# Kernel tuning notes

Measured on AMD Instinct MI355X. Metric: run time of the kernel, lower is better.

Reference implementation:

```python
import jax, jax.numpy as jnp
import numpy as np

N = 50000      # nodes
E = 800000     # edges (avg degree 16)
G = 8          # graphs in batch
D = 128        # in/hidden feats
C = 10         # classes


def setup_inputs() -> dict:
    key = jax.random.key(0)
    ks = jax.random.split(key, 9)
    x = jax.random.normal(ks[0], (N, D), dtype=jnp.float32)
    edge_index = jax.random.randint(ks[1], (2, E), 0, N)
    node2graph = jnp.sort(jax.random.randint(ks[2], (N,), 0, G))
    s = 1.0 / np.sqrt(D)
    W1 = jax.random.normal(ks[3], (D, D), dtype=jnp.float32) * s
    b1 = jnp.zeros((D,), jnp.float32)
    W2 = jax.random.normal(ks[4], (D, D), dtype=jnp.float32) * s
    b2 = jnp.zeros((D,), jnp.float32)
    Wl = jax.random.normal(ks[5], (D, C), dtype=jnp.float32) * s
    bl = jnp.zeros((C,), jnp.float32)
    return {"x": x, "edge_index": edge_index, "node2graph": node2graph,
            "W1": W1, "b1": b1, "W2": W2, "b2": b2, "Wl": Wl, "bl": bl}


def _graph_conv(h, src, dst, out_isqrt, in_isqrt, W, b):
    # DGL GraphConv, norm='both': D_in^{-1/2} A D_out^{-1/2} (h W) + b
    h = (h * out_isqrt[:, None]) @ W
    agg = jax.ops.segment_sum(h[src], dst, num_segments=N)  # SpMM gather/scatter
    return agg * in_isqrt[:, None] + b


def reference(x, edge_index, node2graph, W1, b1, W2, b2, Wl, bl):
    src, dst = edge_index[0], edge_index[1]
    ones_e = jnp.ones((E,), jnp.float32)
    out_deg = jnp.clip(jax.ops.segment_sum(ones_e, src, num_segments=N), 1.0)
    in_deg = jnp.clip(jax.ops.segment_sum(ones_e, dst, num_segments=N), 1.0)
    out_isqrt = jax.lax.rsqrt(out_deg)
    in_isqrt = jax.lax.rsqrt(in_deg)

    h = jax.nn.relu(_graph_conv(x, src, dst, out_isqrt, in_isqrt, W1, b1))
    h = jax.nn.relu(_graph_conv(h, src, dst, out_isqrt, in_isqrt, W2, b2))

    # AvgPooling: per-graph mean of node features
    sums = jax.ops.segment_sum(h, node2graph, num_segments=G)
    counts = jnp.clip(jax.ops.segment_sum(jnp.ones((N,), jnp.float32), node2graph, num_segments=G), 1.0)
    hg = sums / counts[:, None]

    logits = hg @ Wl + bl
    return jax.nn.softmax(logits, axis=1)
```

## Files before the change

### kernel.cpp

```cpp
#include <hip/hip_runtime.h>
#include <stdint.h>

#define FD 128
#define NG 8
#define NC 10
#define MAXB 1024
#define CHUNK 4096
#define BFPAD 16

typedef __attribute__((ext_vector_type(8))) short bf16x8;
typedef __attribute__((ext_vector_type(4))) float f32x4;
typedef __attribute__((ext_vector_type(2))) float f32x2;

__device__ __forceinline__ float bf2f(uint16_t u){
    union { uint32_t i; float f; } v; v.i = ((uint32_t)u) << 16; return v.f;
}
__device__ __forceinline__ uint16_t f2bf(float f){
    union { float f; uint32_t i; } v; v.f = f;
    uint32_t r = v.i + 0x7fff + ((v.i >> 16) & 1);
    return (uint16_t)(r >> 16);
}

#if __has_builtin(__builtin_amdgcn_cvt_pk_f32_fp8) && __has_builtin(__builtin_amdgcn_cvt_pk_fp8_f32)
__device__ __forceinline__ f32x2 fp8lo2f(uint32_t p){
    return __builtin_amdgcn_cvt_pk_f32_fp8((int)p, false);
}
__device__ __forceinline__ f32x2 fp8hi2f(uint32_t p){
    return __builtin_amdgcn_cvt_pk_f32_fp8((int)p, true);
}
__device__ __forceinline__ uint32_t pk4fp8(float a, float b, float c, float d){
    int u = 0;
    u = __builtin_amdgcn_cvt_pk_fp8_f32(a, b, u, false);
    u = __builtin_amdgcn_cvt_pk_fp8_f32(c, d, u, true);
    return (uint32_t)u;
}
#else
__device__ __forceinline__ float fp8tof(uint32_t b){
    union { uint32_t i; float f; } v;
    v.i = ((b & 0x7f) << 20) | ((b & 0x80) << 24);
    return v.f * 0x1p120f;
}
__device__ __forceinline__ f32x2 fp8lo2f(uint32_t p){
    return (f32x2){fp8tof(p & 0xff), fp8tof((p >> 8) & 0xff)};
}
__device__ __forceinline__ f32x2 fp8hi2f(uint32_t p){
    return (f32x2){fp8tof((p >> 16) & 0xff), fp8tof((p >> 24) & 0xff)};
}
__device__ __forceinline__ uint32_t f2fp8(float f){
    union { float f; uint32_t i; } v; v.f = f;
    uint32_t s = (v.i >> 24) & 0x80;
    float a = fabsf(f);
    if (a < 0x1p-10f) return s;
    if (a > 448.f) return s | 0x7e;
    v.f = a;
    uint32_t r = v.i + 0x7ffff + ((v.i >> 20) & 1);
    int e = (int)(r >> 23) - 127 + 7;
    uint32_t m = (r >> 20) & 7;
    if (e <= 0){
        uint32_t q = (uint32_t)(a * 512.f + 0.5f);
        return s | (q > 7 ? 8 : q);
    }
    if (e > 15) return s | 0x7e;
    return s | ((uint32_t)e << 3) | m;
}
__device__ __forceinline__ uint32_t pk4fp8(float a, float b, float c, float d){
    return (uint32_t)f2fp8(a) | ((uint32_t)f2fp8(b)<<8) |
           ((uint32_t)f2fp8(c)<<16) | ((uint32_t)f2fp8(d)<<24);
}
#endif

__global__ __launch_bounds__(256) void k_prep(const float* __restrict__ W1,
        const float* __restrict__ W2, uint16_t* Wf1, uint16_t* Wf2,
        int N, int B, int* __restrict__ deg_out, int* __restrict__ bucket_fill,
        float* __restrict__ pool){
    int t = threadIdx.x;
    int id = blockIdx.x*256 + t;
    {
        int w = id >> 14;
        int r = id & 16383;
        int j = r & 7, frag = r >> 3;
        int lane = frag & 63, t2 = frag >> 6;
        int n = t2 & 7, kk = t2 >> 3;
        int k = kk*32 + (lane>>4)*8 + j;
        int col = n*16 + (lane&15);
        float v = (w ? W2 : W1)[k*128 + col];
        (w ? Wf2 : Wf1)[r] = f2bf(v);
    }
    for (int i = id; i < N; i += 32768) deg_out[i] = 0;
    for (int i = id; i < B*BFPAD; i += 32768) bucket_fill[i] = 0;
    if (id < NG*FD) pool[id] = 0.f;
}

__global__ __launch_bounds__(1024) void k_gemm_scatter(const int* __restrict__ ei,
        int E, int B, int shift, int CAP, int C,
        int* __restrict__ bucket_fill, int* __restrict__ deg_out,
        uint32_t* __restrict__ tempD,
        const float* __restrict__ X, const uint16_t* __restrict__ Wf,
        uint8_t* __restrict__ out8, int N){
    int t = threadIdx.x;
    if (blockIdx.x < C){
        __shared__ int hc[MAXB];
        __shared__ int hb_[MAXB];
        int c = blockIdx.x;
        for (int i=t;i<B;i+=1024) hc[i]=0;
        __syncthreads();
        int e0 = c*CHUNK, e1 = min(E, e0+CHUNK);
        int ss[4], dd[4], pl[4];
        #pragma unroll
        for (int k=0;k<4;k++){
            int e = e0 + t + k*1024;
            bool ok = e < e1;
            int s = ok ? ei[e]   : 0;
            int d = ok ? ei[E+e] : -1;
            ss[k] = s; dd[k] = d; pl[k] = 0;
            if (ok){
                pl[k] = atomicAdd(&hc[d>>shift], 1);
                atomicAdd(&deg_out[s], 1);
            }
        }
        __syncthreads();
        for (int i=t;i<B;i+=1024){
            int cn = hc[i];
            hb_[i] = cn ? atomicAdd(&bucket_fill[i*BFPAD], cn) : 0;
        }
        __syncthreads();
        int lmask = (1<<shift) - 1;
        #pragma unroll
        for (int k=0;k<4;k++){
            int d = dd[k];
            if (d >= 0){
                int b = d >> shift;
                int p = hb_[b] + pl[k];
                if (p < CAP)
                    tempD[(size_t)b*CAP + p] = ((uint32_t)(d & lmask) << 20) | (uint32_t)ss[k];
            }
        }
        return;
    }
    int wave = t>>6, lane = t&63, quad = lane>>4, low = lane&15;
    int rowA  = (blockIdx.x - C)*256 + wave*16 + low;
    int rowAc = min(rowA, N-1);
    const float* arow = X + (size_t)rowAc*FD;
    bf16x8 ah[4];
    #pragma unroll
    for (int kk=0;kk<4;kk++){
        f32x4 f0 = *(const f32x4*)(arow + kk*32 + quad*8);
        f32x4 f1 = *(const f32x4*)(arow + kk*32 + quad*8 + 4);
        #pragma unroll
        for (int j=0;j<4;j++) ah[kk][j]   = (short)f2bf(f0[j]);
        #pragma unroll
        for (int j=0;j<4;j++) ah[kk][j+4] = (short)f2bf(f1[j]);
    }
    f32x4 acc[8];
    #pragma unroll
    for (int n=0;n<8;n++) acc[n] = (f32x4){0.f,0.f,0.f,0.f};
    #pragma unroll
    for (int kk=0;kk<4;kk++){
        #pragma unroll
        for (int n=0;n<8;n++){
            bf16x8 bh = *(const bf16x8*)(Wf + ((size_t)((kk*8+n)*64 + lane))*8);
            acc[n] = __builtin_amdgcn_mfma_f32_16x16x32_bf16(bh, ah[kk], acc[n], 0, 0, 0);
        }
    }
    if (rowA < N){
        uint8_t* orow = out8 + (size_t)rowA*FD;
        #pragma unroll
        for (int n=0;n<8;n++){
            uint32_t pk = pk4fp8(acc[n][0], acc[n][1], acc[n][2], acc[n][3]);
            *(uint32_t*)(orow + n*16 + quad*4) = pk;
        }
    }
}

__global__ __launch_bounds__(256) void k_build(const uint32_t* __restrict__ tempD,
        const int* __restrict__ bucket_fill, const int* __restrict__ deg_out,
        int B, int shift, int N, int CAP,
        int* __restrict__ row_off, int* __restrict__ deg_in,
        float* __restrict__ isqo, int* __restrict__ csr){
    __shared__ int cnt_[MAXB];
    __shared__ int off_[MAXB];
    int b = blockIdx.x, t = threadIdx.x;
    int range = 1<<shift, nb0 = b<<shift;
    int fill = min(bucket_fill[b*BFPAD], CAP);
    const uint32_t* seg = tempD + (size_t)b*CAP;
    for (int i=t;i<range;i+=256) cnt_[i]=0;
    __syncthreads();
    for (int i=t;i<fill;i+=256)
        atomicAdd(&cnt_[seg[i]>>20], 1);
    __syncthreads();
    if (range == 64){
        if (t < 64){
            int v = cnt_[t];
            int inc = v;
            #pragma unroll
            for (int o=1;o<64;o<<=1){
                int u = __shfl_up(inc, o);
                if (t >= o) inc += u;
            }
            off_[t] = inc - v;
        }
    } else if (t == 0){
        int run = 0;
        for (int i=0;i<range;i++){ off_[i]=run; run+=cnt_[i]; }
    }
    __syncthreads();
    int base = b*CAP;
    for (int i=t;i<range;i+=256){
        int node = nb0 + i;
        if (node < N){
            row_off[node] = base + off_[i];
            deg_in[node]  = cnt_[i];
            isqo[node]    = rsqrtf((float)max(deg_out[node], 1));
        }
    }
    __syncthreads();
    int* csrb = csr + (size_t)base;
    for (int i=t;i<fill;i+=256){
        uint32_t v = seg[i];
        int p = atomicAdd(&off_[v>>20], 1);
        csrb[p] = (int)(v & 0xFFFFFu);
    }
}

__device__ __forceinline__ void spmm_row(const uint2* __restrict__ tp,
        const int* __restrict__ csr_src, const float* __restrict__ isqo,
        int e0, int e1, int l, int qb,
        f32x2& a01, f32x2& a23, f32x2& a45, f32x2& a67){
    for (int base = e0; base < e1; base += 16){
        int my = 0;
        if (base + l < e1) my = csr_src[base + l];
        int cnt = min(16, e1 - base);
        for (int j0 = 0; j0 < cnt; j0 += 8){
            int ss[8];
            #pragma unroll
            for (int k=0;k<8;k++)
                ss[k] = __shfl(my, qb + min(j0 + k, cnt-1));
            uint2 p[8]; float w[8];
            #pragma unroll
            for (int k=0;k<8;k++)
                p[k] = tp[(size_t)ss[k]*16 + l];
            #pragma unroll
            for (int k=0;k<8;k++)
                w[k] = isqo[ss[k]];
            #pragma unroll
            for (int k=0;k<8;k++){
                if (j0 + k < cnt){
                    a01 += fp8lo2f(p[k].x)*w[k]; a23 += fp8hi2f(p[k].x)*w[k];
                    a45 += fp8lo2f(p[k].y)*w[k]; a67 += fp8hi2f(p[k].y)*w[k];
                }
            }
        }
    }
}

__global__ __launch_bounds__(256) void k_spmm_gemm(const uint8_t* __restrict__ tmp8,
        const int* __restrict__ row_off, const int* __restrict__ deg_in,
        const int* __restrict__ csr_src, const float* __restrict__ isqo,
        const float* __restrict__ bias, const uint16_t* __restrict__ Wf,
        uint8_t* __restrict__ out8, int N){
    __shared__ __align__(16) uint16_t hsrow[64][136];
    int tid = threadIdx.x;
    int l = tid & 15, qid = tid >> 4, qb = (tid & 63) & 48;
    const uint2* tp = (const uint2*)tmp8;
    f32x4 bv0 = *(const f32x4*)(bias + l*8);
    f32x4 bv1 = *(const f32x4*)(bias + l*8 + 4);
    #pragma unroll
    for (int i = 0; i < 4; i++){
        int rowL = qid*4 + i;
        int node = blockIdx.x*64 + rowL;
        int e0 = 0, e1 = 0;
        if (node < N){ e0 = row_off[node]; e1 = e0 + deg_in[node]; }
        f32x2 a01={0.f,0.f}, a23={0.f,0.f}, a45={0.f,0.f}, a67={0.f,0.f};
        spmm_row(tp, csr_src, isqo, e0, e1, l, qb, a01, a23, a45, a67);
        float isq = rsqrtf((float)max(e1 - e0, 1));
        float r0 = fmaxf(a01.x*isq + bv0[0], 0.f);
        float r1 = fmaxf(a01.y*isq + bv0[1], 0.f);
        float r2 = fmaxf(a23.x*isq + bv0[2], 0.f);
        float r3 = fmaxf(a23.y*isq + bv0[3], 0.f);
        float r4 = fmaxf(a45.x*isq + bv1[0], 0.f);
        float r5 = fmaxf(a45.y*isq + bv1[1], 0.f);
        float r6 = fmaxf(a67.x*isq + bv1[2], 0.f);
        float r7 = fmaxf(a67.y*isq + bv1[3], 0.f);
        uint4 o;
        o.x = (uint32_t)f2bf(r0) | ((uint32_t)f2bf(r1) << 16);
        o.y = (uint32_t)f2bf(r2) | ((uint32_t)f2bf(r3) << 16);
        o.z = (uint32_t)f2bf(r4) | ((uint32_t)f2bf(r5) << 16);
        o.w = (uint32_t)f2bf(r6) | ((uint32_t)f2bf(r7) << 16);
        if (node >= N) o = (uint4){0u,0u,0u,0u};
        *(uint4*)(&hsrow[rowL][l*8]) = o;
    }
    __syncthreads();
    int wave = tid>>6, lane = tid&63, quad = lane>>4, low = lane&15;
    int rowL = wave*16 + low;
    int rowA = blockIdx.x*64 + rowL;
    bf16x8 ah[4];
    #pragma unroll
    for (int kk=0;kk<4;kk++)
        ah[kk] = *(const bf16x8*)(&hsrow[rowL][kk*32 + quad*8]);
    f32x4 acc[8];
    #pragma unroll
    for (int n=0;n<8;n++) acc[n] = (f32x4){0.f,0.f,0.f,0.f};
    #pragma unroll
    for (int kk=0;kk<4;kk++){
        #pragma unroll
        for (int n=0;n<8;n++){
            bf16x8 bh = *(const bf16x8*)(Wf + ((size_t)((kk*8+n)*64 + lane))*8);
            acc[n] = __builtin_amdgcn_mfma_f32_16x16x32_bf16(bh, ah[kk], acc[n], 0, 0, 0);
        }
    }
    if (rowA < N){
        uint8_t* orow = out8 + (size_t)rowA*FD;
        #pragma unroll
        for (int n=0;n<8;n++){
            uint32_t pk = pk4fp8(acc[n][0], acc[n][1], acc[n][2], acc[n][3]);
            *(uint32_t*)(orow + n*16 + quad*4) = pk;
        }
    }
}

__global__ __launch_bounds__(256) void k_spmm_pool(const uint8_t* __restrict__ tmp8,
        const int* __restrict__ row_off, const int* __restrict__ deg_in,
        const int* __restrict__ csr_src, const float* __restrict__ isqo,
        const float* __restrict__ bias, const int* __restrict__ n2g,
        float* __restrict__ pool, int N){
    __shared__ float sacc[NG*FD];
    int tid = threadIdx.x;
    for (int i = tid; i < NG*FD; i += 256) sacc[i] = 0.f;
    __syncthreads();
    int l = tid & 15, qid = tid >> 4, qb = (tid & 63) & 48;
    const uint2* tp = (const uint2*)tmp8;
    f32x4 bv0 = *(const f32x4*)(bias + l*8);
    f32x4 bv1 = *(const f32x4*)(bias + l*8 + 4);
    int rg = -1;
    float racc[8];
    #pragma unroll
    for (int j=0;j<8;j++) racc[j] = 0.f;
    #pragma unroll
    for (int i = 0; i < 4; i++){
        int node = blockIdx.x*64 + qid*4 + i;
        if (node < N){
            int e0 = row_off[node], e1 = e0 + deg_in[node];
            f32x2 a01={0.f,0.f}, a23={0.f,0.f}, a45={0.f,0.f}, a67={0.f,0.f};
            spmm_row(tp, csr_src, isqo, e0, e1, l, qb, a01, a23, a45, a67);
            float isq = rsqrtf((float)max(e1 - e0, 1));
            float r[8];
            r[0] = fmaxf(a01.x*isq + bv0[0], 0.f);
            r[1] = fmaxf(a01.y*isq + bv0[1], 0.f);
            r[2] = fmaxf(a23.x*isq + bv0[2], 0.f);
            r[3] = fmaxf(a23.y*isq + bv0[3], 0.f);
            r[4] = fmaxf(a45.x*isq + bv1[0], 0.f);
            r[5] = fmaxf(a45.y*isq + bv1[1], 0.f);
            r[6] = fmaxf(a67.x*isq + bv1[2], 0.f);
            r[7] = fmaxf(a67.y*isq + bv1[3], 0.f);
            int g = n2g[node];
            if (g != rg){
                if (rg >= 0){
                    #pragma unroll
                    for (int j=0;j<8;j++) atomicAdd(&sacc[rg*FD + l*8 + j], racc[j]);
                }
                rg = g;
                #pragma unroll
                for (int j=0;j<8;j++) racc[j] = 0.f;
            }
            #pragma unroll
            for (int j=0;j<8;j++) racc[j] += r[j];
        }
    }
    if (rg >= 0){
        #pragma unroll
        for (int j=0;j<8;j++) atomicAdd(&sacc[rg*FD + l*8 + j], racc[j]);
    }
    __syncthreads();
    for (int i = tid; i < NG*FD; i += 256){
        float v = sacc[i];
        if (v != 0.f) atomicAdd(&pool[i], v);
    }
}

__global__ __launch_bounds__(128) void k_final(const float* __restrict__ pool,
        const int* __restrict__ n2g, int N, const float* __restrict__ Wl,
        const float* __restrict__ bl, float* __restrict__ out){
    __shared__ int ub[NG+1];
    __shared__ float logits[NG][NC];
    int t = threadIdx.x;
    if (t <= NG){
        int lo = 0, hi = N;
        while (lo < hi){ int mid = (lo+hi)>>1; if (n2g[mid] < t) lo = mid+1; else hi = mid; }
        ub[t] = lo;
    }
    __syncthreads();
    if (t < NG*NC){
        int g = t/NC, c = t%NC;
        float cnt = (float)max(ub[g+1]-ub[g], 1);
        float inv = 1.f/cnt;
        float acc = bl[c];
        for (int d=0; d<FD; d++)
            acc += pool[g*FD+d]*inv * Wl[d*NC+c];
        logits[g][c] = acc;
    }
    __syncthreads();
    if (t < NG*NC){
        int g = t/NC, c = t%NC;
        float m = -1e30f;
        for (int i=0;i<NC;i++) m = fmaxf(m, logits[g][i]);
        float ssum = 0.f;
        for (int i=0;i<NC;i++) ssum += expf(logits[g][i]-m);
        out[t] = expf(logits[g][c]-m)/ssum;
    }
}

extern "C" void kernel_launch(void* const* d_in, const int* in_sizes, int n_in,
                              void* d_out, int out_size, void* d_ws, size_t ws_size,
                              hipStream_t stream) {
    const float* x   = (const float*)d_in[0];
    const int*   ei  = (const int*)d_in[1];
    const int*   n2g = (const int*)d_in[2];
    const float* W1  = (const float*)d_in[3];
    const float* b1  = (const float*)d_in[4];
    const float* W2  = (const float*)d_in[5];
    const float* b2  = (const float*)d_in[6];
    const float* Wl  = (const float*)d_in[7];
    const float* bl  = (const float*)d_in[8];
    float* outp = (float*)d_out;

    int N = in_sizes[2];
    int E = in_sizes[1] / 2;

    int shift = 6;
    while ((((N + (1<<shift) - 1) >> shift) > MAXB) && shift < 10) shift++;
    int B = (N + (1<<shift) - 1) >> shift;
    int C = (E + CHUNK - 1) / CHUNK;
    int meanFill = (int)(((long long)E << shift) / (N > 0 ? N : 1)) + 1;
    int CAP = 4096;
    while (CAP < 4*meanFill) CAP <<= 1;

    char* w = (char*)d_ws;
    size_t off = 0;
    auto alloc = [&](size_t bytes)->char*{ char* p = w + off; off += (bytes + 255) & ~(size_t)255; return p; };
    float*    pool        = (float*)alloc((size_t)NG*FD*4);
    int*      deg_out     = (int*)alloc((size_t)N*4);
    int*      deg_in      = (int*)alloc((size_t)N*4);
    int*      row_off     = (int*)alloc((size_t)N*4);
    float*    isqo        = (float*)alloc((size_t)N*4);
    int*      bucket_fill = (int*)alloc((size_t)MAXB*BFPAD*4);
    uint16_t* Wf1         = (uint16_t*)alloc(16384*2);
    uint16_t* Wf2         = (uint16_t*)alloc(16384*2);
    uint32_t* tempD       = (uint32_t*)alloc((size_t)B*CAP*4);
    int*      csr         = (int*)alloc((size_t)B*CAP*4);
    uint8_t*  tmp8        = (uint8_t*)alloc((size_t)N*FD);
    uint8_t*  tmp8b       = (uint8_t*)alloc((size_t)N*FD);
    (void)ws_size;

    int gb2 = (N + 255)/256;
    int gb  = (N + 63)/64;

    k_prep        <<<128,      256,  0, stream>>>(W1, W2, Wf1, Wf2, N, B, deg_out, bucket_fill, pool);
    k_gemm_scatter<<<C + gb2,  1024, 0, stream>>>(ei, E, B, shift, CAP, C,
                                                  bucket_fill, deg_out, tempD,
                                                  x, Wf1, tmp8, N);
    k_build       <<<B,        256,  0, stream>>>(tempD, bucket_fill, deg_out, B, shift, N, CAP,
                                                  row_off, deg_in, isqo, csr);
    k_spmm_gemm   <<<gb,       256,  0, stream>>>(tmp8,  row_off, deg_in, csr, isqo, b1, Wf2, tmp8b, N);
    k_spmm_pool   <<<gb,       256,  0, stream>>>(tmp8b, row_off, deg_in, csr, isqo, b2, n2g, pool, N);
    k_final       <<<1,        128,  0, stream>>>(pool, n2g, N, Wl, bl, outp);
}
```

Measured before the change: 220.6 us.

## Stage edge buckets in LDS for coalesced writes; bucket out-degree via source buckets

Edge scatter blocks now group each chunk's edges by destination bucket in LDS with padded offsets and write them to global memory as 16-byte vectors, replacing scattered 4-byte writes. Out-degree counting moves from global atomics on deg_out to a second set of blocks that bucket 16-bit source-local IDs, which k_build then counts in LDS. The layer-2 out-degree normalisation is folded into the fp8 output of k_spmm_gemm, so k_spmm_pool skips the per-edge isqo gather. The cost is extra block-wide prefix scans with many syncthreads, padding sentinels that must be filtered, and a smaller CAP that raises the risk of bucket overflow.

```diff
diff --git a/kernel.cpp b/kernel.cpp
--- a/kernel.cpp
+++ b/kernel.cpp
@@ -6,7 +6,7 @@
 #define NC 10
 #define MAXB 1024
 #define CHUNK 4096
-#define BFPAD 16
+#define BFPAD 4
 
 typedef __attribute__((ext_vector_type(8))) short bf16x8;
 typedef __attribute__((ext_vector_type(4))) float f32x4;
@@ -71,7 +71,7 @@
 
 __global__ __launch_bounds__(256) void k_prep(const float* __restrict__ W1,
         const float* __restrict__ W2, uint16_t* Wf1, uint16_t* Wf2,
-        int N, int B, int* __restrict__ deg_out, int* __restrict__ bucket_fill,
+        int B, int* __restrict__ bfD, int* __restrict__ bfS,
         float* __restrict__ pool){
     int t = threadIdx.x;
     int id = blockIdx.x*256 + t;
@@ -86,59 +86,121 @@
         float v = (w ? W2 : W1)[k*128 + col];
         (w ? Wf2 : Wf1)[r] = f2bf(v);
     }
-    for (int i = id; i < N; i += 32768) deg_out[i] = 0;
-    for (int i = id; i < B*BFPAD; i += 32768) bucket_fill[i] = 0;
+    for (int i = id; i < B*BFPAD; i += 32768){ bfD[i] = 0; bfS[i] = 0; }
     if (id < NG*FD) pool[id] = 0.f;
 }
 
 __global__ __launch_bounds__(1024) void k_gemm_scatter(const int* __restrict__ ei,
         int E, int B, int shift, int CAP, int C,
-        int* __restrict__ bucket_fill, int* __restrict__ deg_out,
-        uint32_t* __restrict__ tempD,
+        int* __restrict__ bfD, int* __restrict__ bfS,
+        uint32_t* __restrict__ tempD, uint16_t* __restrict__ tempS,
         const float* __restrict__ X, const uint16_t* __restrict__ Wf,
         uint8_t* __restrict__ out8, int N){
+    __shared__ __align__(16) char lds[45056];
     int t = threadIdx.x;
-    if (blockIdx.x < C){
-        __shared__ int hc[MAXB];
-        __shared__ int hb_[MAXB];
+    int lmask = (1<<shift) - 1;
+    if ((int)blockIdx.x < C){
+        uint32_t* pay = (uint32_t*)lds;
+        int* cnt  = (int*)(lds + 7168*4);
+        int* off  = cnt  + MAXB;
+        int* resv = off  + MAXB;
+        int* scr  = resv + MAXB;
+        for (int i=t;i<7168;i+=1024) pay[i] = 0xFFFFFFFFu;
+        for (int i=t;i<B;i+=1024) cnt[i] = 0;
+        __syncthreads();
         int c = blockIdx.x;
-        for (int i=t;i<B;i+=1024) hc[i]=0;
-        __syncthreads();
         int e0 = c*CHUNK, e1 = min(E, e0+CHUNK);
-        int ss[4], dd[4], pl[4];
+        int bb[4], pl[4]; uint32_t val[4];
         #pragma unroll
         for (int k=0;k<4;k++){
             int e = e0 + t + k*1024;
-            bool ok = e < e1;
-            int s = ok ? ei[e]   : 0;
-            int d = ok ? ei[E+e] : -1;
-            ss[k] = s; dd[k] = d; pl[k] = 0;
-            if (ok){
-                pl[k] = atomicAdd(&hc[d>>shift], 1);
-                atomicAdd(&deg_out[s], 1);
-            }
-        }
-        __syncthreads();
-        for (int i=t;i<B;i+=1024){
-            int cn = hc[i];
-            hb_[i] = cn ? atomicAdd(&bucket_fill[i*BFPAD], cn) : 0;
-        }
-        __syncthreads();
-        int lmask = (1<<shift) - 1;
+            bb[k] = -1;
+            if (e < e1){
+                int s = ei[e], d = ei[E+e];
+                int b = d >> shift;
+                bb[k] = b; val[k] = ((uint32_t)(d & lmask) << 20) | (uint32_t)s;
+                pl[k] = atomicAdd(&cnt[b], 1);
+            }
+        }
+        __syncthreads();
+        int v = (t < B) ? ((cnt[t]+3) & ~3) : 0;
+        scr[t] = v; __syncthreads();
+        for (int o=1;o<1024;o<<=1){ int u=(t>=o)?scr[t-o]:0; __syncthreads(); scr[t]+=u; __syncthreads(); }
+        if (t < B) off[t] = scr[t] - v;
+        __syncthreads();
+        int totalPad = scr[1023];
+        #pragma unroll
+        for (int k=0;k<4;k++)
+            if (bb[k] >= 0) pay[off[bb[k]] + pl[k]] = val[k];
+        for (int b=t;b<B;b+=1024){
+            int pc = (cnt[b]+3) & ~3;
+            resv[b] = pc ? atomicAdd(&bfD[b*BFPAD], pc) : 0;
+        }
+        __syncthreads();
+        for (int g=t; g < (totalPad>>2); g += 1024){
+            int pos = g << 2;
+            int lo = 0, hi = B-1;
+            while (lo < hi){ int mid=(lo+hi+1)>>1; if (off[mid] <= pos) lo = mid; else hi = mid-1; }
+            int rel = resv[lo] + (pos - off[lo]);
+            if (rel + 4 <= CAP){
+                uint4 w4 = *(const uint4*)&pay[pos];
+                *(uint4*)&tempD[(size_t)lo*CAP + rel] = w4;
+            }
+        }
+        return;
+    }
+    if ((int)blockIdx.x < 2*C){
+        uint16_t* pay = (uint16_t*)lds;
+        int* cnt  = (int*)(lds + 11264*2);
+        int* off  = cnt  + MAXB;
+        int* resv = off  + MAXB;
+        int* scr  = resv + MAXB;
+        for (int i=t;i<11264;i+=1024) pay[i] = 0xFFFF;
+        for (int i=t;i<B;i+=1024) cnt[i] = 0;
+        __syncthreads();
+        int c = blockIdx.x - C;
+        int e0 = c*CHUNK, e1 = min(E, e0+CHUNK);
+        int bb[4], pl[4]; uint16_t val[4];
         #pragma unroll
         for (int k=0;k<4;k++){
-            int d = dd[k];
-            if (d >= 0){
-                int b = d >> shift;
-                int p = hb_[b] + pl[k];
-                if (p < CAP)
-                    tempD[(size_t)b*CAP + p] = ((uint32_t)(d & lmask) << 20) | (uint32_t)ss[k];
+            int e = e0 + t + k*1024;
+            bb[k] = -1;
+            if (e < e1){
+                int s = ei[e];
+                int b = s >> shift;
+                bb[k] = b; val[k] = (uint16_t)(s & lmask);
+                pl[k] = atomicAdd(&cnt[b], 1);
+            }
+        }
+        __syncthreads();
+        int v = (t < B) ? ((cnt[t]+7) & ~7) : 0;
+        scr[t] = v; __syncthreads();
+        for (int o=1;o<1024;o<<=1){ int u=(t>=o)?scr[t-o]:0; __syncthreads(); scr[t]+=u; __syncthreads(); }
+        if (t < B) off[t] = scr[t] - v;
+        __syncthreads();
+        int totalPad = scr[1023];
+        #pragma unroll
+        for (int k=0;k<4;k++)
+            if (bb[k] >= 0) pay[off[bb[k]] + pl[k]] = val[k];
+        for (int b=t;b<B;b+=1024){
+            int pc = (cnt[b]+7) & ~7;
+            resv[b] = pc ? atomicAdd(&bfS[b*BFPAD], pc) : 0;
+        }
+        __syncthreads();
+        for (int g=t; g < (totalPad>>3); g += 1024){
+            int pos = g << 3;
+            int lo = 0, hi = B-1;
+            while (lo < hi){ int mid=(lo+hi+1)>>1; if (off[mid] <= pos) lo = mid; else hi = mid-1; }
+            int rel = resv[lo] + (pos - off[lo]);
+            if (rel + 8 <= CAP){
+                uint4 w4 = *(const uint4*)&pay[pos];
+                *(uint4*)&tempS[(size_t)lo*CAP + rel] = w4;
             }
         }
         return;
     }
     int wave = t>>6, lane = t&63, quad = lane>>4, low = lane&15;
-    int rowA  = (blockIdx.x - C)*256 + wave*16 + low;
+    int rowA  = (blockIdx.x - 2*C)*256 + wave*16 + low;
     int rowAc = min(rowA, N-1);
     const float* arow = X + (size_t)rowAc*FD;
     bf16x8 ah[4];
@@ -173,7 +235,8 @@
 }
 
 __global__ __launch_bounds__(256) void k_build(const uint32_t* __restrict__ tempD,
-        const int* __restrict__ bucket_fill, const int* __restrict__ deg_out,
+        const uint16_t* __restrict__ tempS,
+        const int* __restrict__ bfD, const int* __restrict__ bfS,
         int B, int shift, int N, int CAP,
         int* __restrict__ row_off, int* __restrict__ deg_in,
         float* __restrict__ isqo, int* __restrict__ csr){
@@ -181,12 +244,14 @@
     __shared__ int off_[MAXB];
     int b = blockIdx.x, t = threadIdx.x;
     int range = 1<<shift, nb0 = b<<shift;
-    int fill = min(bucket_fill[b*BFPAD], CAP);
+    int fill = min(bfD[b*BFPAD], CAP);
     const uint32_t* seg = tempD + (size_t)b*CAP;
     for (int i=t;i<range;i+=256) cnt_[i]=0;
     __syncthreads();
-    for (int i=t;i<fill;i+=256)
-        atomicAdd(&cnt_[seg[i]>>20], 1);
+    for (int i=t;i<fill;i+=256){
+        int loc = (int)(seg[i] >> 20);
+        if (loc < range) atomicAdd(&cnt_[loc], 1);
+    }
     __syncthreads();
     if (range == 64){
         if (t < 64){
@@ -210,18 +275,35 @@
         if (node < N){
             row_off[node] = base + off_[i];
             deg_in[node]  = cnt_[i];
-            isqo[node]    = rsqrtf((float)max(deg_out[node], 1));
         }
     }
     __syncthreads();
     int* csrb = csr + (size_t)base;
     for (int i=t;i<fill;i+=256){
         uint32_t v = seg[i];
-        int p = atomicAdd(&off_[v>>20], 1);
-        csrb[p] = (int)(v & 0xFFFFFu);
-    }
-}
-
+        int loc = (int)(v >> 20);
+        if (loc < range){
+            int p = atomicAdd(&off_[loc], 1);
+            csrb[p] = (int)(v & 0xFFFFFu);
+        }
+    }
+    __syncthreads();
+    for (int i=t;i<range;i+=256) cnt_[i]=0;
+    __syncthreads();
+    int fillS = min(bfS[b*BFPAD], CAP);
+    const uint16_t* segS = tempS + (size_t)b*CAP;
+    for (int i=t;i<fillS;i+=256){
+        int v = (int)segS[i];
+        if (v < range) atomicAdd(&cnt_[v], 1);
+    }
+    __syncthreads();
+    for (int i=t;i<range;i+=256){
+        int node = nb0 + i;
+        if (node < N) isqo[node] = rsqrtf((float)max(cnt_[i], 1));
+    }
+}
+
+template<bool WSCALE>
 __device__ __forceinline__ void spmm_row(const uint2* __restrict__ tp,
         const int* __restrict__ csr_src, const float* __restrict__ isqo,
         int e0, int e1, int l, int qb,
@@ -239,14 +321,20 @@
             #pragma unroll
             for (int k=0;k<8;k++)
                 p[k] = tp[(size_t)ss[k]*16 + l];
-            #pragma unroll
-            for (int k=0;k<8;k++)
-                w[k] = isqo[ss[k]];
+            if (WSCALE){
+                #pragma unroll
+                for (int k=0;k<8;k++) w[k] = isqo[ss[k]];
+            }
             #pragma unroll
             for (int k=0;k<8;k++){
                 if (j0 + k < cnt){
-                    a01 += fp8lo2f(p[k].x)*w[k]; a23 += fp8hi2f(p[k].x)*w[k];
-                    a45 += fp8lo2f(p[k].y)*w[k]; a67 += fp8hi2f(p[k].y)*w[k];
+                    if (WSCALE){
+                        a01 += fp8lo2f(p[k].x)*w[k]; a23 += fp8hi2f(p[k].x)*w[k];
+                        a45 += fp8lo2f(p[k].y)*w[k]; a67 += fp8hi2f(p[k].y)*w[k];
+                    } else {
+                        a01 += fp8lo2f(p[k].x); a23 += fp8hi2f(p[k].x);
+                        a45 += fp8lo2f(p[k].y); a67 += fp8hi2f(p[k].y);
+                    }
                 }
             }
         }
@@ -271,7 +359,7 @@
         int e0 = 0, e1 = 0;
         if (node < N){ e0 = row_off[node]; e1 = e0 + deg_in[node]; }
         f32x2 a01={0.f,0.f}, a23={0.f,0.f}, a45={0.f,0.f}, a67={0.f,0.f};
-        spmm_row(tp, csr_src, isqo, e0, e1, l, qb, a01, a23, a45, a67);
+        spmm_row<true>(tp, csr_src, isqo, e0, e1, l, qb, a01, a23, a45, a67);
         float isq = rsqrtf((float)max(e1 - e0, 1));
         float r0 = fmaxf(a01.x*isq + bv0[0], 0.f);
         float r1 = fmaxf(a01.y*isq + bv0[1], 0.f);
@@ -309,10 +397,11 @@
         }
     }
     if (rowA < N){
+        float sc = isqo[rowA];
         uint8_t* orow = out8 + (size_t)rowA*FD;
         #pragma unroll
         for (int n=0;n<8;n++){
-            uint32_t pk = pk4fp8(acc[n][0], acc[n][1], acc[n][2], acc[n][3]);
+            uint32_t pk = pk4fp8(acc[n][0]*sc, acc[n][1]*sc, acc[n][2]*sc, acc[n][3]*sc);
             *(uint32_t*)(orow + n*16 + quad*4) = pk;
         }
     }
@@ -320,7 +409,7 @@
 
 __global__ __launch_bounds__(256) void k_spmm_pool(const uint8_t* __restrict__ tmp8,
         const int* __restrict__ row_off, const int* __restrict__ deg_in,
-        const int* __restrict__ csr_src, const float* __restrict__ isqo,
+        const int* __restrict__ csr_src,
         const float* __restrict__ bias, const int* __restrict__ n2g,
         float* __restrict__ pool, int N){
     __shared__ float sacc[NG*FD];
@@ -341,7 +430,7 @@
         if (node < N){
             int e0 = row_off[node], e1 = e0 + deg_in[node];
             f32x2 a01={0.f,0.f}, a23={0.f,0.f}, a45={0.f,0.f}, a67={0.f,0.f};
-            spmm_row(tp, csr_src, isqo, e0, e1, l, qb, a01, a23, a45, a67);
+            spmm_row<false>(tp, csr_src, nullptr, e0, e1, l, qb, a01, a23, a45, a67);
             float isq = rsqrtf((float)max(e1 - e0, 1));
             float r[8];
             r[0] = fmaxf(a01.x*isq + bv0[0], 0.f);
@@ -432,35 +521,36 @@
     int C = (E + CHUNK - 1) / CHUNK;
     int meanFill = (int)(((long long)E << shift) / (N > 0 ? N : 1)) + 1;
     int CAP = 4096;
-    while (CAP < 4*meanFill) CAP <<= 1;
+    while (CAP < 3*meanFill) CAP <<= 1;
 
     char* w = (char*)d_ws;
     size_t off = 0;
     auto alloc = [&](size_t bytes)->char*{ char* p = w + off; off += (bytes + 255) & ~(size_t)255; return p; };
-    float*    pool        = (float*)alloc((size_t)NG*FD*4);
-    int*      deg_out     = (int*)alloc((size_t)N*4);
-    int*      deg_in      = (int*)alloc((size_t)N*4);
-    int*      row_off     = (int*)alloc((size_t)N*4);
-    float*    isqo        = (float*)alloc((size_t)N*4);
-    int*      bucket_fill = (int*)alloc((size_t)MAXB*BFPAD*4);
-    uint16_t* Wf1         = (uint16_t*)alloc(16384*2);
-    uint16_t* Wf2         = (uint16_t*)alloc(16384*2);
-    uint32_t* tempD       = (uint32_t*)alloc((size_t)B*CAP*4);
-    int*      csr         = (int*)alloc((size_t)B*CAP*4);
-    uint8_t*  tmp8        = (uint8_t*)alloc((size_t)N*FD);
-    uint8_t*  tmp8b       = (uint8_t*)alloc((size_t)N*FD);
+    float*    pool    = (float*)alloc((size_t)NG*FD*4);
+    int*      deg_in  = (int*)alloc((size_t)N*4);
+    int*      row_off = (int*)alloc((size_t)N*4);
+    float*    isqo    = (float*)alloc((size_t)N*4);
+    int*      bfD     = (int*)alloc((size_t)MAXB*BFPAD*4);
+    int*      bfS     = (int*)alloc((size_t)MAXB*BFPAD*4);
+    uint16_t* Wf1     = (uint16_t*)alloc(16384*2);
+    uint16_t* Wf2     = (uint16_t*)alloc(16384*2);
+    uint32_t* tempD   = (uint32_t*)alloc((size_t)B*CAP*4);
+    uint16_t* tempS   = (uint16_t*)alloc((size_t)B*CAP*2);
+    int*      csr     = (int*)alloc((size_t)B*CAP*4);
+    uint8_t*  tmp8    = (uint8_t*)alloc((size_t)N*FD);
+    uint8_t*  tmp8b   = (uint8_t*)alloc((size_t)N*FD);
     (void)ws_size;
 
     int gb2 = (N + 255)/256;
     int gb  = (N + 63)/64;
 
-    k_prep        <<<128,      256,  0, stream>>>(W1, W2, Wf1, Wf2, N, B, deg_out, bucket_fill, pool);
-    k_gemm_scatter<<<C + gb2,  1024, 0, stream>>>(ei, E, B, shift, CAP, C,
-                                                  bucket_fill, deg_out, tempD,
-                                                  x, Wf1, tmp8, N);
-    k_build       <<<B,        256,  0, stream>>>(tempD, bucket_fill, deg_out, B, shift, N, CAP,
-                                                  row_off, deg_in, isqo, csr);
-    k_spmm_gemm   <<<gb,       256,  0, stream>>>(tmp8,  row_off, deg_in, csr, isqo, b1, Wf2, tmp8b, N);
-    k_spmm_pool   <<<gb,       256,  0, stream>>>(tmp8b, row_off, deg_in, csr, isqo, b2, n2g, pool, N);
-    k_final       <<<1,        128,  0, stream>>>(pool, n2g, N, Wl, bl, outp);
-}
+    k_prep        <<<128,         256,  0, stream>>>(W1, W2, Wf1, Wf2, B, bfD, bfS, pool);
+    k_gemm_scatter<<<2*C + gb2,   1024, 0, stream>>>(ei, E, B, shift, CAP, C,
+                                                     bfD, bfS, tempD, tempS,
+                                                     x, Wf1, tmp8, N);
+    k_build       <<<B,           256,  0, stream>>>(tempD, tempS, bfD, bfS, B, shift, N, CAP,
+                                                     row_off, deg_in, isqo, csr);
+    k_spmm_gemm   <<<gb,          256,  0, stream>>>(tmp8,  row_off, deg_in, csr, isqo, b1, Wf2, tmp8b, N);
+    k_spmm_pool   <<<gb,          256,  0, stream>>>(tmp8b, row_off, deg_in, csr, b2, n2g, pool, N);
+    k_final       <<<1,           128,  0, stream>>>(pool, n2g, N, Wl, bl, outp);
+}
```

Measured after the change: 197.9 us. 10.3% less time.
